# Performance work log

Hardware: AMD Instinct MI355X
Metric: run time of the kernel (lower is better)

Reference implementation:

```python
import jax, jax.numpy as jnp
import numpy as np

BN_EPS = 1e-5


def setup_inputs() -> dict:
    key = jax.random.key(0)
    ks = jax.random.split(key, 3)
    B, S, C, H, W = 4, 8, 64, 96, 96
    P = 6
    DIM = 768
    x = jax.random.normal(ks[0], (B, S, C, H, W), dtype=jnp.float32)
    conv_w = jax.random.normal(ks[1], (C, C, 3, 3), dtype=jnp.float32) * 0.05
    conv_b = jnp.zeros((C,), dtype=jnp.float32)
    bn_gamma = jnp.ones((C,), dtype=jnp.float32)
    bn_beta = jnp.zeros((C,), dtype=jnp.float32)
    bn_mean = jnp.zeros((C,), dtype=jnp.float32)
    bn_var = jnp.ones((C,), dtype=jnp.float32)
    proj_w = jax.random.normal(ks[2], (DIM, P * P * C), dtype=jnp.float32) * 0.02
    proj_b = jnp.zeros((DIM,), dtype=jnp.float32)
    mask = jnp.ones((P, P), dtype=jnp.float32)
    return {"x": x, "conv_w": conv_w, "conv_b": conv_b,
            "bn_gamma": bn_gamma, "bn_beta": bn_beta,
            "bn_mean": bn_mean, "bn_var": bn_var,
            "proj_w": proj_w, "proj_b": proj_b,
            "mask": mask, "patch_size": P}


def reference(x, conv_w, conv_b, bn_gamma, bn_beta, bn_mean, bn_var,
              proj_w, proj_b, mask, patch_size):
    B, S, C, H, W = x.shape
    p = patch_size
    Cout = conv_w.shape[0]
    # Fuse the per-frame loop: run conv over all B*S frames at once.
    xf = x.reshape(B * S, C, H, W)
    y = jax.lax.conv_general_dilated(
        xf, conv_w, window_strides=(1, 1), padding=[(1, 1), (1, 1)],
        dimension_numbers=("NCHW", "OIHW", "NCHW"))
    y = y + conv_b[None, :, None, None]
    # BatchNorm2d (eval-mode running stats); Dropout2d is identity at eval.
    inv = jax.lax.rsqrt(bn_var + BN_EPS)
    y = (y - bn_mean[None, :, None, None]) * (bn_gamma * inv)[None, :, None, None] \
        + bn_beta[None, :, None, None]
    y = jax.nn.gelu(y, approximate=False)  # torch GELU default = exact erf
    y = y.reshape(B, S, Cout, H, W)
    # Patch extraction, row-major over (l_idx, r_idx) exactly as the loop.
    pr = H // p  # patches per row
    patches = y.reshape(B, S, Cout, pr, p, pr, p).transpose(0, 1, 3, 5, 2, 4, 6)
    patches = patches.reshape(B, S, pr * pr, Cout, p, p) * mask  # [B,S,P,C,p,p]
    # Flatten(start_dim=2 on [B,S,C,p,p]) + Linear + GELU, batched over patches.
    flat = patches.reshape(B, S, pr * pr, Cout * p * p)
    tokens = jax.nn.gelu(
        jnp.einsum("bsnf,df->bsnd", flat, proj_w) + proj_b, approximate=False)
    return tokens, patches
```

## Files before the change

kernel.cpp:

```cpp
#include <hip/hip_runtime.h>
#include <hip/hip_bf16.h>
#include <math.h>


typedef unsigned short u16;
typedef __bf16 bf16x8 __attribute__((ext_vector_type(8)));
typedef float f32x4 __attribute__((ext_vector_type(4)));

#define NFRM 32
#define CH 64
#define HW 96
#define HWP 98
#define KP 2304
#define DIMN 768
#define MTOK 8192
#define TOKN (MTOK * DIMN)
#define NPAT (MTOK * KP)
#define XHWC_ELEMS ((size_t)NFRM * HWP * HWP * CH)
#define BP_OFF XHWC_ELEMS
#define PW_OFF (BP_OFF + 36864)

static __device__ __forceinline__ u16 f2b(float f) {
  unsigned u = __builtin_bit_cast(unsigned, f);
  u += 0x7fffu + ((u >> 16) & 1u);
  return (u16)(u >> 16);
}
static __device__ __forceinline__ float gelu_f(float x) {
  return 0.5f * x * (1.0f + erff(x * 0.7071067811865476f));
}

__global__ __launch_bounds__(256) void k_transpose(const float* __restrict__ x,
                                                   u16* __restrict__ xhwc) {
  __shared__ u16 tile[96 * 66];
  const int f = blockIdx.x / 96, h = blockIdx.x % 96;
  const int t = threadIdx.x;
  const float* xp = x + (size_t)f * CH * HW * HW + (size_t)h * HW;
#pragma unroll
  for (int k = 0; k < 6; ++k) {
    int e = (k * 256 + t) * 4;
    int ci = e / 96, w = e % 96;
    float4 v = *(const float4*)(xp + (size_t)ci * (HW * HW) + w);
    tile[(w + 0) * 66 + ci] = f2b(v.x);
    tile[(w + 1) * 66 + ci] = f2b(v.y);
    tile[(w + 2) * 66 + ci] = f2b(v.z);
    tile[(w + 3) * 66 + ci] = f2b(v.w);
  }
  __syncthreads();
  u16* op = xhwc + ((size_t)(f * HWP + h + 1) * HWP + 1) * CH;
#pragma unroll
  for (int k = 0; k < 12; ++k) {
    int e2 = (k * 256 + t) * 2;
    int w = e2 >> 6, ci = e2 & 63;
    *(unsigned*)(op + e2) = *(const unsigned*)(&tile[w * 66 + ci]);
  }
}

__global__ __launch_bounds__(256) void k_bpack(const float* __restrict__ w,
                                               u16* __restrict__ bp) {
  int e = blockIdx.x * 256 + threadIdx.x;
  int co = e / 576, r = e - co * 576, tap = r >> 6, ci = r & 63;
  bp[e] = f2b(w[(co * 64 + ci) * 9 + tap]);
}

__global__ __launch_bounds__(256) void k_pw(const float* __restrict__ pw,
                                            u16* __restrict__ dst) {
  int e = (blockIdx.x * 256 + threadIdx.x) * 4;
  float4 v = *(const float4*)(pw + e);
  ushort4 o;
  o.x = f2b(v.x); o.y = f2b(v.y); o.z = f2b(v.z); o.w = f2b(v.w);
  *(ushort4*)(dst + e) = o;
}

__global__ __launch_bounds__(256) void k_conv(
    const u16* __restrict__ xhwc, const u16* __restrict__ bw,
    const float* __restrict__ cb, const float* __restrict__ gma,
    const float* __restrict__ bta, const float* __restrict__ mu,
    const float* __restrict__ var, const float* __restrict__ msk,
    float* __restrict__ pout) {
  __shared__ u16 As[128 * 72];
  __shared__ u16 Bs[64 * 72];
  const int f = blockIdx.x / 72;
  const int m0 = (blockIdx.x % 72) * 128;
  const int t = threadIdx.x;
  const int wv = t >> 6, l = t & 63, quad = l >> 4, lm = l & 15;

  const int r = t >> 1, c0 = (t & 1) * 32;
  const int mg = m0 + r;
  const int np = mg / 36, ii = mg - np * 36;
  const int hb = (np >> 4) * 6 + ii / 6;
  const int wb = (np & 15) * 6 + (ii % 6);
  const u16* xf = xhwc + (size_t)f * (HWP * HWP * CH);
  const int bco = t >> 2, bc = (t & 3) * 16;

  f32x4 acc[2][4];
#pragma unroll
  for (int s = 0; s < 2; ++s)
#pragma unroll
    for (int u = 0; u < 4; ++u) acc[s][u] = (f32x4){0.f, 0.f, 0.f, 0.f};

  for (int tap = 0; tap < 9; ++tap) {
    const int di = tap / 3, dj = tap - di * 3;
    __syncthreads();
    const u16* src = xf + ((hb + di) * HWP + (wb + dj)) * CH + c0;
    u16* dA = &As[r * 72 + c0];
    *(uint4*)(dA + 0) = *(const uint4*)(src + 0);
    *(uint4*)(dA + 8) = *(const uint4*)(src + 8);
    *(uint4*)(dA + 16) = *(const uint4*)(src + 16);
    *(uint4*)(dA + 24) = *(const uint4*)(src + 24);
    const u16* bsrc = bw + bco * 576 + tap * 64 + bc;
    u16* dB = &Bs[bco * 72 + bc];
    *(uint4*)(dB + 0) = *(const uint4*)(bsrc + 0);
    *(uint4*)(dB + 8) = *(const uint4*)(bsrc + 8);
    __syncthreads();
#pragma unroll
    for (int ks = 0; ks < 2; ++ks) {
      const int ko = ks * 32 + quad * 8;
      bf16x8 a0 = *(const bf16x8*)&As[(wv * 32 + lm) * 72 + ko];
      bf16x8 a1 = *(const bf16x8*)&As[(wv * 32 + 16 + lm) * 72 + ko];
#pragma unroll
      for (int u = 0; u < 4; ++u) {
        bf16x8 b = *(const bf16x8*)&Bs[(u * 16 + lm) * 72 + ko];
        acc[0][u] = __builtin_amdgcn_mfma_f32_16x16x32_bf16(a0, b, acc[0][u], 0, 0, 0);
        acc[1][u] = __builtin_amdgcn_mfma_f32_16x16x32_bf16(a1, b, acc[1][u], 0, 0, 0);
      }
    }
  }
  const int mwb = m0 + wv * 32;
#pragma unroll
  for (int u = 0; u < 4; ++u) {
    const int co = u * 16 + lm;
    const float scv = gma[co] * rsqrtf(var[co] + 1e-5f);
    const float b2v = (cb[co] - mu[co]) * scv + bta[co];
#pragma unroll
    for (int s = 0; s < 2; ++s) {
#pragma unroll
      for (int rg = 0; rg < 4; ++rg) {
        const int ml = mwb + s * 16 + quad * 4 + rg;
        const int n = ml / 36, jj = ml - n * 36;
        float v = acc[s][u][rg] * scv + b2v;
        v = gelu_f(v) * msk[jj];
        pout[((size_t)(f * 256 + n) * 64 + co) * 36 + jj] = v;
      }
    }
  }
}

__global__ __launch_bounds__(256) void k_cvt(const float* __restrict__ pat,
                                             u16* __restrict__ abf) {
  int e = (blockIdx.x * 256 + threadIdx.x) * 4;
  float4 v = *(const float4*)(pat + e);
  ushort4 o;
  o.x = f2b(v.x); o.y = f2b(v.y); o.z = f2b(v.z); o.w = f2b(v.w);
  *(ushort4*)(abf + e) = o;
}

__global__ __launch_bounds__(256) void k_gemm(const u16* __restrict__ A,
                                              const u16* __restrict__ Bt,
                                              const float* __restrict__ pb,
                                              float* __restrict__ out) {
  __shared__ u16 As[128 * 40];
  __shared__ u16 Bs[64 * 40];
  const int bn = blockIdx.x % 12, bm = blockIdx.x / 12;
  const int m0 = bm * 128, n0 = bn * 64;
  const int t = threadIdx.x, wv = t >> 6, l = t & 63, quad = l >> 4, lm = l & 15;
  const int ar = t >> 2, ac = (t & 3) * 8;

  f32x4 acc[2][4];
#pragma unroll
  for (int s = 0; s < 2; ++s)
#pragma unroll
    for (int u = 0; u < 4; ++u) acc[s][u] = (f32x4){0.f, 0.f, 0.f, 0.f};

  for (int k0 = 0; k0 < KP; k0 += 32) {
    __syncthreads();
    *(uint4*)&As[ar * 40 + ac] = *(const uint4*)&A[(size_t)(m0 + ar) * KP + k0 + ac];
    *(uint4*)&As[(ar + 64) * 40 + ac] =
        *(const uint4*)&A[(size_t)(m0 + ar + 64) * KP + k0 + ac];
    *(uint4*)&Bs[ar * 40 + ac] = *(const uint4*)&Bt[(size_t)(n0 + ar) * KP + k0 + ac];
    __syncthreads();
    const int ko = quad * 8;
    bf16x8 a0 = *(const bf16x8*)&As[(wv * 32 + lm) * 40 + ko];
    bf16x8 a1 = *(const bf16x8*)&As[(wv * 32 + 16 + lm) * 40 + ko];
#pragma unroll
    for (int u = 0; u < 4; ++u) {
      bf16x8 b = *(const bf16x8*)&Bs[(u * 16 + lm) * 40 + ko];
      acc[0][u] = __builtin_amdgcn_mfma_f32_16x16x32_bf16(a0, b, acc[0][u], 0, 0, 0);
      acc[1][u] = __builtin_amdgcn_mfma_f32_16x16x32_bf16(a1, b, acc[1][u], 0, 0, 0);
    }
  }
#pragma unroll
  for (int u = 0; u < 4; ++u) {
    const int n = n0 + u * 16 + lm;
    const float bias = pb[n];
#pragma unroll
    for (int s = 0; s < 2; ++s) {
#pragma unroll
      for (int rg = 0; rg < 4; ++rg) {
        const int m = m0 + wv * 32 + s * 16 + quad * 4 + rg;
        out[(size_t)m * DIMN + n] = gelu_f(acc[s][u][rg] + bias);
      }
    }
  }
}

extern "C" void kernel_launch(void* const* d_in, const int* in_sizes, int n_in,
                              void* d_out, int out_size, void* d_ws, size_t ws_size,
                              hipStream_t stream) {
  const float* x = (const float*)d_in[0];
  const float* conv_w = (const float*)d_in[1];
  const float* conv_b = (const float*)d_in[2];
  const float* bn_gamma = (const float*)d_in[3];
  const float* bn_beta = (const float*)d_in[4];
  const float* bn_mean = (const float*)d_in[5];
  const float* bn_var = (const float*)d_in[6];
  const float* proj_w = (const float*)d_in[7];
  const float* proj_b = (const float*)d_in[8];
  const float* mask = (const float*)d_in[9];
  float* out = (float*)d_out;
  float* patches = out + TOKN;
  u16* ws = (u16*)d_ws;
  u16* xhwc = ws;
  u16* bp = ws + BP_OFF;
  u16* pw = ws + PW_OFF;

  hipMemsetAsync(d_ws, 0, XHWC_ELEMS * sizeof(u16), stream);
  k_transpose<<<NFRM * HW, 256, 0, stream>>>(x, xhwc);
  k_bpack<<<144, 256, 0, stream>>>(conv_w, bp);
  k_pw<<<1728, 256, 0, stream>>>(proj_w, pw);
  k_conv<<<NFRM * 72, 256, 0, stream>>>(xhwc, bp, conv_b, bn_gamma, bn_beta,
                                        bn_mean, bn_var, mask, patches);
  k_cvt<<<18432, 256, 0, stream>>>(patches, xhwc);
  k_gemm<<<64 * 12, 256, 0, stream>>>(xhwc, pw, proj_b, out);
}
```

Baseline: 327.5 us.

## Halo-tiled conv, border-only padding zeroing, fused fp32→bf16 load in 128x128 GEMM

The conv kernel now loads a 4-row halo of the padded HWC input into shared memory once per block and computes all nine taps from it. Weight fragments are read directly from global memory, which removes the per-tap global reloads and barriers. The full-buffer memset is replaced by a small kernel that writes only the padding border. The separate fp32→bf16 conversion pass over patches is dropped: the projection GEMM reads fp32 patches, converts them while staging into LDS, and uses a larger 128x128 tile with K-step 64. The border kernel writes only 4 of every 8 channels per slot, so it relies on the workspace already being zero there.

```diff
diff --git a/kernel.cpp b/kernel.cpp
--- a/kernel.cpp
+++ b/kernel.cpp
@@ -6,6 +6,7 @@
 typedef unsigned short u16;
 typedef __bf16 bf16x8 __attribute__((ext_vector_type(8)));
 typedef float f32x4 __attribute__((ext_vector_type(4)));
+typedef u16 u16x8 __attribute__((ext_vector_type(8)));
 
 #define NFRM 32
 #define CH 64
@@ -15,7 +16,6 @@
 #define DIMN 768
 #define MTOK 8192
 #define TOKN (MTOK * DIMN)
-#define NPAT (MTOK * KP)
 #define XHWC_ELEMS ((size_t)NFRM * HWP * HWP * CH)
 #define BP_OFF XHWC_ELEMS
 #define PW_OFF (BP_OFF + 36864)
@@ -27,6 +27,18 @@
 }
 static __device__ __forceinline__ float gelu_f(float x) {
   return 0.5f * x * (1.0f + erff(x * 0.7071067811865476f));
+}
+
+__global__ __launch_bounds__(256) void k_zero(u16* __restrict__ xhwc) {
+  int id = blockIdx.x * 256 + threadIdx.x;
+  int p = id >> 3, cs = id & 7;
+  int f = p / 388, bp = p - f * 388;
+  int h, w;
+  if (bp < 98) { h = 0; w = bp; }
+  else if (bp < 196) { h = 97; w = bp - 98; }
+  else { int q = bp - 196; h = 1 + (q >> 1); w = (q & 1) ? 97 : 0; }
+  ushort4 z = {0, 0, 0, 0};
+  *(ushort4*)(xhwc + ((size_t)(f * HWP + h) * HWP + w) * CH + cs * 8) = z;
 }
 
 __global__ __launch_bounds__(256) void k_transpose(const float* __restrict__ x,
@@ -77,129 +89,145 @@
     const float* __restrict__ bta, const float* __restrict__ mu,
     const float* __restrict__ var, const float* __restrict__ msk,
     float* __restrict__ pout) {
-  __shared__ u16 As[128 * 72];
-  __shared__ u16 Bs[64 * 72];
-  const int f = blockIdx.x / 72;
-  const int m0 = (blockIdx.x % 72) * 128;
+  __shared__ u16 halo[4 * 98 * 72];
+  const int f = blockIdx.x / 48;
+  const int h0 = (blockIdx.x % 48) * 2;
   const int t = threadIdx.x;
   const int wv = t >> 6, l = t & 63, quad = l >> 4, lm = l & 15;
-
-  const int r = t >> 1, c0 = (t & 1) * 32;
-  const int mg = m0 + r;
-  const int np = mg / 36, ii = mg - np * 36;
-  const int hb = (np >> 4) * 6 + ii / 6;
-  const int wb = (np & 15) * 6 + (ii % 6);
   const u16* xf = xhwc + (size_t)f * (HWP * HWP * CH);
-  const int bco = t >> 2, bc = (t & 3) * 16;
-
-  f32x4 acc[2][4];
-#pragma unroll
-  for (int s = 0; s < 2; ++s)
-#pragma unroll
-    for (int u = 0; u < 4; ++u) acc[s][u] = (f32x4){0.f, 0.f, 0.f, 0.f};
-
+
+#pragma unroll
+  for (int it = 0; it < 13; ++it) {
+    int c = it * 256 + t;
+    if (c < 3136) {
+      int hr = c / 784, rem = c - hr * 784;
+      int w = rem >> 3, cs = rem & 7;
+      *(uint4*)(halo + (hr * 98 + w) * 72 + cs * 8) =
+          *(const uint4*)(xf + ((size_t)(h0 + hr) * HWP + w) * CH + cs * 8);
+    }
+  }
+  __syncthreads();
+
+  const int hr_out = wv >> 1;
+  const int wbase = (wv & 1) * 48;
+
+  f32x4 acc[3][4];
+#pragma unroll
+  for (int mt = 0; mt < 3; ++mt)
+#pragma unroll
+    for (int u = 0; u < 4; ++u) acc[mt][u] = (f32x4){0.f, 0.f, 0.f, 0.f};
+
+#pragma unroll
   for (int tap = 0; tap < 9; ++tap) {
     const int di = tap / 3, dj = tap - di * 3;
-    __syncthreads();
-    const u16* src = xf + ((hb + di) * HWP + (wb + dj)) * CH + c0;
-    u16* dA = &As[r * 72 + c0];
-    *(uint4*)(dA + 0) = *(const uint4*)(src + 0);
-    *(uint4*)(dA + 8) = *(const uint4*)(src + 8);
-    *(uint4*)(dA + 16) = *(const uint4*)(src + 16);
-    *(uint4*)(dA + 24) = *(const uint4*)(src + 24);
-    const u16* bsrc = bw + bco * 576 + tap * 64 + bc;
-    u16* dB = &Bs[bco * 72 + bc];
-    *(uint4*)(dB + 0) = *(const uint4*)(bsrc + 0);
-    *(uint4*)(dB + 8) = *(const uint4*)(bsrc + 8);
-    __syncthreads();
-#pragma unroll
-    for (int ks = 0; ks < 2; ++ks) {
-      const int ko = ks * 32 + quad * 8;
-      bf16x8 a0 = *(const bf16x8*)&As[(wv * 32 + lm) * 72 + ko];
-      bf16x8 a1 = *(const bf16x8*)&As[(wv * 32 + 16 + lm) * 72 + ko];
-#pragma unroll
-      for (int u = 0; u < 4; ++u) {
-        bf16x8 b = *(const bf16x8*)&Bs[(u * 16 + lm) * 72 + ko];
-        acc[0][u] = __builtin_amdgcn_mfma_f32_16x16x32_bf16(a0, b, acc[0][u], 0, 0, 0);
-        acc[1][u] = __builtin_amdgcn_mfma_f32_16x16x32_bf16(a1, b, acc[1][u], 0, 0, 0);
+    bf16x8 bfr[2][4];
+#pragma unroll
+    for (int ks = 0; ks < 2; ++ks)
+#pragma unroll
+      for (int u = 0; u < 4; ++u)
+        bfr[ks][u] = *(const bf16x8*)(bw + (u * 16 + lm) * 576 + tap * 64 +
+                                      ks * 32 + quad * 8);
+#pragma unroll
+    for (int mt = 0; mt < 3; ++mt) {
+      const int base = ((hr_out + di) * 98 + wbase + mt * 16 + lm + dj) * 72;
+#pragma unroll
+      for (int ks = 0; ks < 2; ++ks) {
+        bf16x8 a = *(const bf16x8*)(halo + base + ks * 32 + quad * 8);
+#pragma unroll
+        for (int u = 0; u < 4; ++u)
+          acc[mt][u] =
+              __builtin_amdgcn_mfma_f32_16x16x32_bf16(a, bfr[ks][u], acc[mt][u], 0, 0, 0);
       }
     }
   }
-  const int mwb = m0 + wv * 32;
+
+  const int hpx = h0 + hr_out;
+  const int hd = hpx / 6, hm = hpx - hd * 6;
 #pragma unroll
   for (int u = 0; u < 4; ++u) {
     const int co = u * 16 + lm;
     const float scv = gma[co] * rsqrtf(var[co] + 1e-5f);
     const float b2v = (cb[co] - mu[co]) * scv + bta[co];
 #pragma unroll
-    for (int s = 0; s < 2; ++s) {
+    for (int mt = 0; mt < 3; ++mt) {
 #pragma unroll
       for (int rg = 0; rg < 4; ++rg) {
-        const int ml = mwb + s * 16 + quad * 4 + rg;
-        const int n = ml / 36, jj = ml - n * 36;
-        float v = acc[s][u][rg] * scv + b2v;
-        v = gelu_f(v) * msk[jj];
-        pout[((size_t)(f * 256 + n) * 64 + co) * 36 + jj] = v;
+        const int wpx = wbase + mt * 16 + quad * 4 + rg;
+        const int wd = wpx / 6, wm = wpx - wd * 6;
+        const int np = hd * 16 + wd, ii = hm * 6 + wm;
+        float v = acc[mt][u][rg] * scv + b2v;
+        v = gelu_f(v) * msk[ii];
+        pout[((size_t)(f * 256 + np) * 64 + co) * 36 + ii] = v;
       }
     }
   }
 }
 
-__global__ __launch_bounds__(256) void k_cvt(const float* __restrict__ pat,
-                                             u16* __restrict__ abf) {
-  int e = (blockIdx.x * 256 + threadIdx.x) * 4;
-  float4 v = *(const float4*)(pat + e);
-  ushort4 o;
-  o.x = f2b(v.x); o.y = f2b(v.y); o.z = f2b(v.z); o.w = f2b(v.w);
-  *(ushort4*)(abf + e) = o;
-}
-
-__global__ __launch_bounds__(256) void k_gemm(const u16* __restrict__ A,
+__global__ __launch_bounds__(256) void k_gemm(const float* __restrict__ A,
                                               const u16* __restrict__ Bt,
                                               const float* __restrict__ pb,
                                               float* __restrict__ out) {
-  __shared__ u16 As[128 * 40];
-  __shared__ u16 Bs[64 * 40];
-  const int bn = blockIdx.x % 12, bm = blockIdx.x / 12;
-  const int m0 = bm * 128, n0 = bn * 64;
+  __shared__ u16 As[128 * 72];
+  __shared__ u16 Bs[128 * 72];
+  const int bm = blockIdx.x / 6, bn = blockIdx.x % 6;
+  const int m0 = bm * 128, n0 = bn * 128;
   const int t = threadIdx.x, wv = t >> 6, l = t & 63, quad = l >> 4, lm = l & 15;
-  const int ar = t >> 2, ac = (t & 3) * 8;
-
-  f32x4 acc[2][4];
-#pragma unroll
-  for (int s = 0; s < 2; ++s)
-#pragma unroll
-    for (int u = 0; u < 4; ++u) acc[s][u] = (f32x4){0.f, 0.f, 0.f, 0.f};
-
-  for (int k0 = 0; k0 < KP; k0 += 32) {
+  const int wm = wv & 1, wn = wv >> 1;
+  const int ar = t >> 1, half = (t & 1) * 32;
+
+  f32x4 acc[4][4];
+#pragma unroll
+  for (int mt = 0; mt < 4; ++mt)
+#pragma unroll
+    for (int ut = 0; ut < 4; ++ut) acc[mt][ut] = (f32x4){0.f, 0.f, 0.f, 0.f};
+
+  for (int k0 = 0; k0 < KP; k0 += 64) {
     __syncthreads();
-    *(uint4*)&As[ar * 40 + ac] = *(const uint4*)&A[(size_t)(m0 + ar) * KP + k0 + ac];
-    *(uint4*)&As[(ar + 64) * 40 + ac] =
-        *(const uint4*)&A[(size_t)(m0 + ar + 64) * KP + k0 + ac];
-    *(uint4*)&Bs[ar * 40 + ac] = *(const uint4*)&Bt[(size_t)(n0 + ar) * KP + k0 + ac];
+    const float* asrc = A + (size_t)(m0 + ar) * KP + k0 + half;
+    u16* adst = As + ar * 72 + half;
+#pragma unroll
+    for (int c = 0; c < 4; ++c) {
+      float4 v0 = *(const float4*)(asrc + c * 8);
+      float4 v1 = *(const float4*)(asrc + c * 8 + 4);
+      u16x8 o;
+      o[0] = f2b(v0.x); o[1] = f2b(v0.y); o[2] = f2b(v0.z); o[3] = f2b(v0.w);
+      o[4] = f2b(v1.x); o[5] = f2b(v1.y); o[6] = f2b(v1.z); o[7] = f2b(v1.w);
+      *(u16x8*)(adst + c * 8) = o;
+    }
+    const u16* bsrc = Bt + (size_t)(n0 + ar) * KP + k0 + half;
+    u16* bdst = Bs + ar * 72 + half;
+#pragma unroll
+    for (int c = 0; c < 4; ++c)
+      *(uint4*)(bdst + c * 8) = *(const uint4*)(bsrc + c * 8);
     __syncthreads();
-    const int ko = quad * 8;
-    bf16x8 a0 = *(const bf16x8*)&As[(wv * 32 + lm) * 40 + ko];
-    bf16x8 a1 = *(const bf16x8*)&As[(wv * 32 + 16 + lm) * 40 + ko];
-#pragma unroll
-    for (int u = 0; u < 4; ++u) {
-      bf16x8 b = *(const bf16x8*)&Bs[(u * 16 + lm) * 40 + ko];
-      acc[0][u] = __builtin_amdgcn_mfma_f32_16x16x32_bf16(a0, b, acc[0][u], 0, 0, 0);
-      acc[1][u] = __builtin_amdgcn_mfma_f32_16x16x32_bf16(a1, b, acc[1][u], 0, 0, 0);
-    }
-  }
-#pragma unroll
-  for (int u = 0; u < 4; ++u) {
-    const int n = n0 + u * 16 + lm;
+#pragma unroll
+    for (int ks = 0; ks < 2; ++ks) {
+      bf16x8 af[4], bf[4];
+#pragma unroll
+      for (int mt = 0; mt < 4; ++mt)
+        af[mt] = *(const bf16x8*)&As[(wm * 64 + mt * 16 + lm) * 72 + ks * 32 + quad * 8];
+#pragma unroll
+      for (int ut = 0; ut < 4; ++ut)
+        bf[ut] = *(const bf16x8*)&Bs[(wn * 64 + ut * 16 + lm) * 72 + ks * 32 + quad * 8];
+#pragma unroll
+      for (int mt = 0; mt < 4; ++mt)
+#pragma unroll
+        for (int ut = 0; ut < 4; ++ut)
+          acc[mt][ut] =
+              __builtin_amdgcn_mfma_f32_16x16x32_bf16(af[mt], bf[ut], acc[mt][ut], 0, 0, 0);
+    }
+  }
+#pragma unroll
+  for (int ut = 0; ut < 4; ++ut) {
+    const int n = n0 + wn * 64 + ut * 16 + lm;
     const float bias = pb[n];
 #pragma unroll
-    for (int s = 0; s < 2; ++s) {
+    for (int mt = 0; mt < 4; ++mt)
 #pragma unroll
       for (int rg = 0; rg < 4; ++rg) {
-        const int m = m0 + wv * 32 + s * 16 + quad * 4 + rg;
-        out[(size_t)m * DIMN + n] = gelu_f(acc[s][u][rg] + bias);
+        const int m = m0 + wm * 64 + mt * 16 + quad * 4 + rg;
+        out[(size_t)m * DIMN + n] = gelu_f(acc[mt][ut][rg] + bias);
       }
-    }
   }
 }
 
@@ -223,12 +251,11 @@
   u16* bp = ws + BP_OFF;
   u16* pw = ws + PW_OFF;
 
-  hipMemsetAsync(d_ws, 0, XHWC_ELEMS * sizeof(u16), stream);
+  k_zero<<<388, 256, 0, stream>>>(xhwc);
   k_transpose<<<NFRM * HW, 256, 0, stream>>>(x, xhwc);
   k_bpack<<<144, 256, 0, stream>>>(conv_w, bp);
   k_pw<<<1728, 256, 0, stream>>>(proj_w, pw);
-  k_conv<<<NFRM * 72, 256, 0, stream>>>(xhwc, bp, conv_b, bn_gamma, bn_beta,
+  k_conv<<<NFRM * 48, 256, 0, stream>>>(xhwc, bp, conv_b, bn_gamma, bn_beta,
                                         bn_mean, bn_var, mask, patches);
-  k_cvt<<<18432, 256, 0, stream>>>(patches, xhwc);
-  k_gemm<<<64 * 12, 256, 0, stream>>>(xhwc, pw, proj_b, out);
-}
+  k_gemm<<<64 * 6, 256, 0, stream>>>(patches, pw, proj_b, out);
+}
```

New measurement: 406.9 us. 1.24x slower.
